# Optimization experiments

Hardware: AMD Instinct MI355X
Metric: run time of the kernel (lower is better)

Reference implementation:

```python
import jax, jax.numpy as jnp
import numpy as np

N_HEADS = 16
DIMS = 1024
HEAD_SIZE = DIMS // N_HEADS


def setup_inputs() -> dict:
    key = jax.random.key(0)
    k1, k2, k3, k4, k5 = jax.random.split(key, 5)
    x = jax.random.normal(k1, (1, 4096, DIMS), dtype=jnp.float32)
    s = 1.0 / np.sqrt(DIMS)
    w_qkv = jax.random.uniform(k2, (3 * DIMS, DIMS), jnp.float32, -s, s)
    b_qkv = jax.random.uniform(k3, (3 * DIMS,), jnp.float32, -s, s)
    w_o = jax.random.uniform(k4, (DIMS, DIMS), jnp.float32, -s, s)
    b_o = jax.random.uniform(k5, (DIMS,), jnp.float32, -s, s)
    return {"x": x, "w_qkv": w_qkv, "b_qkv": b_qkv, "w_o": w_o, "b_o": b_o,
            "causal_mask": 1}


def reference(x, w_qkv, b_qkv, w_o, b_o, causal_mask):
    B, S, D = x.shape
    qkv = x @ w_qkv.T + b_qkv                      # [B,S,3D]
    q, k, v = jnp.split(qkv, 3, axis=-1)
    def heads(t):
        return t.reshape(B, S, N_HEADS, HEAD_SIZE).transpose(0, 2, 1, 3)  # [B,H,S,hd]
    q, k, v = heads(q), heads(k), heads(v)
    scores = jnp.einsum("bhsd,bhtd->bhst", q, k)   # [B,H,S,S]
    if causal_mask:
        tri = jnp.triu(jnp.ones((S, S), dtype=bool), k=1)
        scores = jnp.where(tri, -jnp.inf, scores)  # mask BEFORE scale, as in torch code
    scores = scores / np.sqrt(HEAD_SIZE)
    weights = jax.nn.softmax(scores, axis=-1)
    out = jnp.einsum("bhst,bhtd->bhsd", weights, v)  # [B,H,S,hd]
    out = out.transpose(0, 2, 1, 3).reshape(B, S, D)
    return out @ w_o.T + b_o
```

## Files before the change

### kernel.cpp

```cpp
#include <hip/hip_runtime.h>
#include <hip/hip_bf16.h>
#include <stdint.h>

typedef __attribute__((ext_vector_type(8))) short short8;
typedef __attribute__((ext_vector_type(4))) float f32x4;
typedef __attribute__((ext_vector_type(16))) float f32x16;
typedef __attribute__((ext_vector_type(2))) unsigned int uint2u;
typedef __hip_bfloat16 bf16;

#define S_LEN 4096
#define DMODEL 1024
#define NH 16
#define HD 64
#define QSCALE 0.1803368801111f

static __device__ inline uint2 pack4(float4 v) {
  union { uint2 u; bf16 h[4]; } p;
  p.h[0] = (bf16)v.x; p.h[1] = (bf16)v.y; p.h[2] = (bf16)v.z; p.h[3] = (bf16)v.w;
  return p.u;
}

static __device__ inline uint32_t pack2(float a, float b) {
  union { uint32_t u; bf16 h[2]; } p;
  p.h[0] = (bf16)a; p.h[1] = (bf16)b;
  return p.u;
}

static __device__ inline float b2f(short s) {
  union { short s; bf16 h; } u; u.s = s; return (float)u.h;
}

static __device__ inline void gload_lds16(const bf16* g, bf16* l) {
  __builtin_amdgcn_global_load_lds(
      (const __attribute__((address_space(1))) unsigned int*)g,
      (__attribute__((address_space(3))) unsigned int*)l, 16, 0, 0);
}

static __device__ inline int rot_idx(int r, int c) {
  return r * 64 + ((c + ((r & 7) << 3)) & 63);
}

__global__ __launch_bounds__(256)
void cvt_all(const float* __restrict__ x, const float* __restrict__ wq,
             const float* __restrict__ wo, bf16* __restrict__ xb,
             bf16* __restrict__ wqb, bf16* __restrict__ wob) {
  const int nx = S_LEN * DMODEL;
  const int nq = 3 * DMODEL * DMODEL;
  const int no = DMODEL * DMODEL;
  int i = (blockIdx.x * 256 + threadIdx.x) * 4;
  if (i < nx) {
    *(uint2*)(xb + i) = pack4(*(const float4*)(x + i));
  } else if (i < nx + nq) {
    int j = i - nx;
    *(uint2*)(wqb + j) = pack4(*(const float4*)(wq + j));
  } else if (i < nx + nq + no) {
    int j = i - nx - nq;
    *(uint2*)(wob + j) = pack4(*(const float4*)(wo + j));
  }
}

__global__ __launch_bounds__(256)
void gemm_qkv(const bf16* __restrict__ A, const bf16* __restrict__ B,
              const float* __restrict__ bias, bf16* __restrict__ qkv2,
              bf16* __restrict__ vt) {
  const int K = DMODEL;
  __shared__ bf16 sA[128 * 64];
  __shared__ bf16 sB[128 * 64];
  const int tid  = threadIdx.x;
  const int lane = tid & 63;
  const int wave = tid >> 6;
  const int wm = wave >> 1, wn = wave & 1;
  const int tileM = blockIdx.y * 128;
  const int tileN = blockIdx.x * 128;

  const int lrow = lane & 15;
  const int quad = lane >> 4;
  const int kq   = quad * 8;

  f32x4 acc[4][4];
#pragma unroll
  for (int i = 0; i < 4; i++)
#pragma unroll
    for (int j = 0; j < 4; j++) acc[i][j] = (f32x4){0.f, 0.f, 0.f, 0.f};

  const int trl = lane >> 3;
  const int cgl = (((lane & 7) - trl) & 7) << 3;
  const bf16* aP[4];
  const bf16* bP[4];
#pragma unroll
  for (int c = 0; c < 4; c++) {
    int ch = wave * 4 + c;
    aP[c] = A + (size_t)(tileM + ch * 8 + trl) * K + cgl;
    bP[c] = B + (size_t)(tileN + ch * 8 + trl) * K + cgl;
  }

  for (int k0 = 0; k0 < K; k0 += 64) {
    __syncthreads();
#pragma unroll
    for (int c = 0; c < 4; c++) {
      int ch = wave * 4 + c;
      gload_lds16(aP[c] + k0, sA + ch * 512);
      gload_lds16(bP[c] + k0, sB + ch * 512);
    }
    __syncthreads();
#pragma unroll
    for (int ks = 0; ks < 2; ks++) {
      short8 afrag[4], bfrag[4];
#pragma unroll
      for (int mi = 0; mi < 4; mi++)
        afrag[mi] = *(const short8*)(sA + rot_idx(wm * 64 + mi * 16 + lrow, ks * 32 + kq));
#pragma unroll
      for (int ni = 0; ni < 4; ni++)
        bfrag[ni] = *(const short8*)(sB + rot_idx(wn * 64 + ni * 16 + lrow, ks * 32 + kq));
#pragma unroll
      for (int mi = 0; mi < 4; mi++)
#pragma unroll
        for (int ni = 0; ni < 4; ni++)
          acc[mi][ni] = __builtin_amdgcn_mfma_f32_16x16x32_bf16(afrag[mi], bfrag[ni], acc[mi][ni], 0, 0, 0);
    }
  }

#pragma unroll
  for (int ni = 0; ni < 4; ni++) {
    int col = tileN + wn * 64 + ni * 16 + lrow;
    float bv = bias[col];
    if (col < 2 * DMODEL) {
      float sc = (col < DMODEL) ? QSCALE : 1.0f;
#pragma unroll
      for (int mi = 0; mi < 4; mi++) {
        int row0 = tileM + wm * 64 + mi * 16 + quad * 4;
#pragma unroll
        for (int r = 0; r < 4; r++)
          qkv2[(size_t)(row0 + r) * 2048 + col] = (bf16)((acc[mi][ni][r] + bv) * sc);
      }
    } else {
      int cc = col - 2 * DMODEL;
      int hh = cc >> 6, dd = cc & 63;
      bf16* vrow = vt + ((size_t)(hh * 64 + dd)) * S_LEN;
#pragma unroll
      for (int mi = 0; mi < 4; mi++) {
        int row0 = tileM + wm * 64 + mi * 16 + quad * 4;
        float4 v = {acc[mi][ni][0] + bv, acc[mi][ni][1] + bv,
                    acc[mi][ni][2] + bv, acc[mi][ni][3] + bv};
        *(uint2*)(vrow + row0) = pack4(v);
      }
    }
  }
}

__global__ __launch_bounds__(256)
void gemm_oproj(const bf16* __restrict__ A, const bf16* __restrict__ B,
                const float* __restrict__ bias, float* __restrict__ C) {
  const int K = DMODEL, N = DMODEL;
  __shared__ bf16 sA[128 * 64];
  __shared__ bf16 sB[64 * 64];
  const int tid  = threadIdx.x;
  const int lane = tid & 63;
  const int wave = tid >> 6;
  const int wm = wave >> 1, wn = wave & 1;
  const int tileM = blockIdx.y * 128;
  const int tileN = blockIdx.x * 64;

  const int lrow = lane & 15;
  const int quad = lane >> 4;
  const int kq   = quad * 8;

  f32x4 acc[4][2];
#pragma unroll
  for (int i = 0; i < 4; i++)
#pragma unroll
    for (int j = 0; j < 2; j++) acc[i][j] = (f32x4){0.f, 0.f, 0.f, 0.f};

  const int trl = lane >> 3;
  const int cgl = (((lane & 7) - trl) & 7) << 3;
  const bf16* aP[4];
  const bf16* bP[2];
#pragma unroll
  for (int c = 0; c < 4; c++) {
    int ch = wave * 4 + c;
    aP[c] = A + (size_t)(tileM + ch * 8 + trl) * K + cgl;
  }
#pragma unroll
  for (int c = 0; c < 2; c++) {
    int ch = wave * 2 + c;
    bP[c] = B + (size_t)(tileN + ch * 8 + trl) * K + cgl;
  }

  for (int k0 = 0; k0 < K; k0 += 64) {
    __syncthreads();
#pragma unroll
    for (int c = 0; c < 4; c++)
      gload_lds16(aP[c] + k0, sA + (wave * 4 + c) * 512);
#pragma unroll
    for (int c = 0; c < 2; c++)
      gload_lds16(bP[c] + k0, sB + (wave * 2 + c) * 512);
    __syncthreads();
#pragma unroll
    for (int ks = 0; ks < 2; ks++) {
      short8 afrag[4], bfrag[2];
#pragma unroll
      for (int mi = 0; mi < 4; mi++)
        afrag[mi] = *(const short8*)(sA + rot_idx(wm * 64 + mi * 16 + lrow, ks * 32 + kq));
#pragma unroll
      for (int ni = 0; ni < 2; ni++)
        bfrag[ni] = *(const short8*)(sB + rot_idx(wn * 32 + ni * 16 + lrow, ks * 32 + kq));
#pragma unroll
      for (int mi = 0; mi < 4; mi++)
#pragma unroll
        for (int ni = 0; ni < 2; ni++)
          acc[mi][ni] = __builtin_amdgcn_mfma_f32_16x16x32_bf16(afrag[mi], bfrag[ni], acc[mi][ni], 0, 0, 0);
    }
  }

#pragma unroll
  for (int ni = 0; ni < 2; ni++) {
    int col = tileN + wn * 32 + ni * 16 + lrow;
    float bv = bias[col];
#pragma unroll
    for (int mi = 0; mi < 4; mi++) {
      int row0 = tileM + wm * 64 + mi * 16 + quad * 4;
#pragma unroll
      for (int r = 0; r < 4; r++)
        C[(size_t)(row0 + r) * N + col] = acc[mi][ni][r] + bv;
    }
  }
}

__global__ __launch_bounds__(256)
void gemm_qkv_f32(const float* __restrict__ A, const float* __restrict__ B,
                  const float* __restrict__ bias, bf16* __restrict__ qkv2,
                  bf16* __restrict__ vt) {
  const int K = DMODEL;
  __shared__ bf16 sA[128 * 64];
  __shared__ bf16 sB[128 * 64];
  const int tid  = threadIdx.x;
  const int lane = tid & 63;
  const int wave = tid >> 6;
  const int wm = wave >> 1, wn = wave & 1;
  const int tileM = blockIdx.y * 128;
  const int tileN = blockIdx.x * 128;
  const int lrow = lane & 15;
  const int quad = lane >> 4;
  const int kq   = quad * 8;

  f32x4 acc[4][4];
#pragma unroll
  for (int i = 0; i < 4; i++)
#pragma unroll
    for (int j = 0; j < 4; j++) acc[i][j] = (f32x4){0.f, 0.f, 0.f, 0.f};

  const int r0 = tid >> 4;
  const int cc = (tid & 15) * 4;

  for (int k0 = 0; k0 < K; k0 += 64) {
    uint2 ra[8], rb[8];
#pragma unroll
    for (int i = 0; i < 8; i++) {
      int row = r0 + i * 16;
      ra[i] = pack4(*(const float4*)(A + (size_t)(tileM + row) * K + k0 + cc));
      rb[i] = pack4(*(const float4*)(B + (size_t)(tileN + row) * K + k0 + cc));
    }
    __syncthreads();
#pragma unroll
    for (int i = 0; i < 8; i++) {
      int row = r0 + i * 16;
      *(uint2*)(sA + row * 64 + cc) = ra[i];
      *(uint2*)(sB + row * 64 + cc) = rb[i];
    }
    __syncthreads();
#pragma unroll
    for (int ks = 0; ks < 2; ks++) {
      short8 afrag[4], bfrag[4];
#pragma unroll
      for (int mi = 0; mi < 4; mi++)
        afrag[mi] = *(const short8*)(sA + (wm * 64 + mi * 16 + lrow) * 64 + ks * 32 + kq);
#pragma unroll
      for (int ni = 0; ni < 4; ni++)
        bfrag[ni] = *(const short8*)(sB + (wn * 64 + ni * 16 + lrow) * 64 + ks * 32 + kq);
#pragma unroll
      for (int mi = 0; mi < 4; mi++)
#pragma unroll
        for (int ni = 0; ni < 4; ni++)
          acc[mi][ni] = __builtin_amdgcn_mfma_f32_16x16x32_bf16(afrag[mi], bfrag[ni], acc[mi][ni], 0, 0, 0);
    }
  }
#pragma unroll
  for (int ni = 0; ni < 4; ni++) {
    int col = tileN + wn * 64 + ni * 16 + lrow;
    float bv = bias[col];
    if (col < 2 * DMODEL) {
      float sc = (col < DMODEL) ? QSCALE : 1.0f;
#pragma unroll
      for (int mi = 0; mi < 4; mi++) {
        int row0 = tileM + wm * 64 + mi * 16 + quad * 4;
#pragma unroll
        for (int r = 0; r < 4; r++)
          qkv2[(size_t)(row0 + r) * 2048 + col] = (bf16)((acc[mi][ni][r] + bv) * sc);
      }
    } else {
      int c2 = col - 2 * DMODEL;
      int hh = c2 >> 6, dd = c2 & 63;
      bf16* vrow = vt + ((size_t)(hh * 64 + dd)) * S_LEN;
#pragma unroll
      for (int mi = 0; mi < 4; mi++) {
        int row0 = tileM + wm * 64 + mi * 16 + quad * 4;
        float4 v = {acc[mi][ni][0] + bv, acc[mi][ni][1] + bv,
                    acc[mi][ni][2] + bv, acc[mi][ni][3] + bv};
        *(uint2*)(vrow + row0) = pack4(v);
      }
    }
  }
}

__global__ __launch_bounds__(256)
void gemm_oproj_f32w(const bf16* __restrict__ A, const float* __restrict__ B,
                     const float* __restrict__ bias, float* __restrict__ C) {
  const int K = DMODEL, N = DMODEL;
  __shared__ bf16 sA[128 * 64];
  __shared__ bf16 sB[128 * 64];
  const int tid  = threadIdx.x;
  const int lane = tid & 63;
  const int wave = tid >> 6;
  const int wm = wave >> 1, wn = wave & 1;
  const int tileM = blockIdx.y * 128;
  const int tileN = blockIdx.x * 128;
  const int lrow = lane & 15;
  const int quad = lane >> 4;
  const int kq   = quad * 8;

  f32x4 acc[4][4];
#pragma unroll
  for (int i = 0; i < 4; i++)
#pragma unroll
    for (int j = 0; j < 4; j++) acc[i][j] = (f32x4){0.f, 0.f, 0.f, 0.f};

  const int a_r0 = tid >> 3;
  const int a_cc = (tid & 7) * 8;
  const int b_r0 = tid >> 4;
  const int b_cc = (tid & 15) * 4;

  for (int k0 = 0; k0 < K; k0 += 64) {
    uint4 ra[4];
    uint2 rb[8];
#pragma unroll
    for (int i = 0; i < 4; i++)
      ra[i] = *(const uint4*)(A + (size_t)(tileM + a_r0 + i * 32) * K + k0 + a_cc);
#pragma unroll
    for (int i = 0; i < 8; i++)
      rb[i] = pack4(*(const float4*)(B + (size_t)(tileN + b_r0 + i * 16) * K + k0 + b_cc));
    __syncthreads();
#pragma unroll
    for (int i = 0; i < 4; i++)
      *(uint4*)(sA + (a_r0 + i * 32) * 64 + a_cc) = ra[i];
#pragma unroll
    for (int i = 0; i < 8; i++)
      *(uint2*)(sB + (b_r0 + i * 16) * 64 + b_cc) = rb[i];
    __syncthreads();
#pragma unroll
    for (int ks = 0; ks < 2; ks++) {
      short8 afrag[4], bfrag[4];
#pragma unroll
      for (int mi = 0; mi < 4; mi++)
        afrag[mi] = *(const short8*)(sA + (wm * 64 + mi * 16 + lrow) * 64 + ks * 32 + kq);
#pragma unroll
      for (int ni = 0; ni < 4; ni++)
        bfrag[ni] = *(const short8*)(sB + (wn * 64 + ni * 16 + lrow) * 64 + ks * 32 + kq);
#pragma unroll
      for (int mi = 0; mi < 4; mi++)
#pragma unroll
        for (int ni = 0; ni < 4; ni++)
          acc[mi][ni] = __builtin_amdgcn_mfma_f32_16x16x32_bf16(afrag[mi], bfrag[ni], acc[mi][ni], 0, 0, 0);
    }
  }
#pragma unroll
  for (int ni = 0; ni < 4; ni++) {
    int col = tileN + wn * 64 + ni * 16 + lrow;
    float bv = bias[col];
#pragma unroll
    for (int mi = 0; mi < 4; mi++) {
      int row0 = tileM + wm * 64 + mi * 16 + quad * 4;
#pragma unroll
      for (int r = 0; r < 4; r++)
        C[(size_t)(row0 + r) * N + col] = acc[mi][ni][r] + bv;
    }
  }
}

__global__ __launch_bounds__(256, 4)
void attn_kernel(const bf16* __restrict__ qkv2, const bf16* __restrict__ vt,
                 bf16* __restrict__ attn_out, const int* __restrict__ causal_ptr,
                 bf16* __restrict__ p0, bf16* __restrict__ p1,
                 bf16* __restrict__ p2) {
  __shared__ bf16 smem[2][64 * 64];
  __shared__ float lbuf[64];

  const int tid  = threadIdx.x;
  const int lane = tid & 63;
  const int wave = tid >> 6;
  const int qh   = wave >> 1;
  const int kh   = wave & 1;

  const int id   = blockIdx.y * 192 + blockIdx.x;
  const int xcd  = id & 7;
  const int hh   = (id >> 3) & 1;
  const int h    = xcd + (hh << 3);
  const int rest = id >> 4;
  const int rank = rest / 3;
  const int ck   = rest - rank * 3;
  const int qi   = 63 - rank;
  const int qbase = qi * 64;
  const bool causal = (*causal_ptr) != 0;

  const int l31 = lane & 31;
  const int hi  = lane >> 5;
  const int trl = lane >> 3;
  const int cgl = (((lane & 7) - trl) & 7) << 3;

  const bf16* Qb = qkv2 + h * HD;
  const bf16* Kb = qkv2 + DMODEL + h * HD;
  const bf16* Vb = vt + (size_t)(h * HD) * S_LEN;

  bf16* const A = smem[0];
  bf16* const B = smem[1];

  const int Lt  = causal ? (qi + 1) : (S_LEN / 64);
  const int jt0 = (Lt * ck) / 3;
  const int jt1 = (Lt * (ck + 1)) / 3;

  const int wrmin = qbase + qh * 32;
  const int wrmax = wrmin + 31;
  const int q_g   = wrmin + l31;

  if (jt0 < jt1) {
#pragma unroll
    for (int i = 0; i < 2; i++) {
      int ch = wave * 2 + i;
      int trow = ch * 8 + trl;
      gload_lds16(Kb + (size_t)(jt0 * 64 + trow) * 2048 + cgl, A + ch * 512);
      gload_lds16(Vb + (size_t)trow * S_LEN + jt0 * 64 + cgl, B + ch * 512);
    }
  }
  short8 qf[4];
#pragma unroll
  for (int kd = 0; kd < 4; kd++)
    qf[kd] = *(const short8*)(Qb + (size_t)q_g * 2048 + kd * 16 + hi * 8);

  f32x16 oacc[2];
#pragma unroll
  for (int nc = 0; nc < 2; nc++)
#pragma unroll
    for (int e = 0; e < 16; e++) oacc[nc][e] = 0.f;
  float l_st = 0.f;

  __syncthreads();

  for (int jt = jt0; jt < jt1; jt++) {
    const int kbase = jt * 64;
    const int kh32 = kbase + kh * 32;
    const bool live = !(causal && kh32 > wrmax);

    uint32_t pw[2][4];
    if (live) {
      f32x16 sacc;
#pragma unroll
      for (int e = 0; e < 16; e++) sacc[e] = 0.f;
      __builtin_amdgcn_s_setprio(1);
#pragma unroll
      for (int kd = 0; kd < 4; kd++) {
        short8 kf = *(const short8*)(A + rot_idx(kh * 32 + l31, kd * 16 + hi * 8));
        sacc = __builtin_amdgcn_mfma_f32_32x32x16_bf16(kf, qf[kd], sacc, 0, 0, 0);
      }
      __builtin_amdgcn_s_setprio(0);
      const bool nm = causal && (kh32 + 31 > wrmin);
      uint32_t pku[4][2];
      float psum = 0.f;
#pragma unroll
      for (int g = 0; g < 4; g++) {
#pragma unroll
        for (int h2 = 0; h2 < 2; h2++) {
          float v0 = __builtin_amdgcn_exp2f(sacc[g * 4 + h2 * 2]);
          float v1 = __builtin_amdgcn_exp2f(sacc[g * 4 + h2 * 2 + 1]);
          if (nm) {
            int kg = kh32 + g * 8 + hi * 4 + h2 * 2;
            if (kg > q_g)     v0 = 0.f;
            if (kg + 1 > q_g) v1 = 0.f;
          }
          psum += v0 + v1;
          pku[g][h2] = pack2(v0, v1);
        }
      }
      l_st += psum;
#pragma unroll
      for (int c2 = 0; c2 < 2; c2++) {
#pragma unroll
        for (int h2 = 0; h2 < 2; h2++) {
          uint2u sw = __builtin_amdgcn_permlane32_swap(
              pku[2 * c2][h2], pku[2 * c2 + 1][h2], false, false);
          pw[c2][h2]     = sw[0];
          pw[c2][2 + h2] = sw[1];
        }
      }
    }

    __syncthreads();

    if (jt + 1 < jt1) {
      const int kb2 = kbase + 64;
#pragma unroll
      for (int i = 0; i < 2; i++) {
        int ch = wave * 2 + i;
        int trow = ch * 8 + trl;
        gload_lds16(Kb + (size_t)(kb2 + trow) * 2048 + cgl, A + ch * 512);
      }
    }

    if (live) {
      __builtin_amdgcn_s_setprio(1);
#pragma unroll
      for (int c2 = 0; c2 < 2; c2++) {
        if (causal && (kh32 + c2 * 16 > wrmax)) continue;
        union { short8 s; uint32_t u[4]; } pf;
#pragma unroll
        for (int w = 0; w < 4; w++) pf.u[w] = pw[c2][w];
#pragma unroll
        for (int nc = 0; nc < 2; nc++) {
          short8 vf = *(const short8*)(B +
              rot_idx(nc * 32 + l31, (kh * 2 + c2) * 16 + hi * 8));
          oacc[nc] = __builtin_amdgcn_mfma_f32_32x32x16_bf16(pf.s, vf, oacc[nc], 0, 0, 0);
        }
      }
      __builtin_amdgcn_s_setprio(0);
    }

    __syncthreads();

    if (jt + 1 < jt1) {
      const int kb2 = kbase + 64;
#pragma unroll
      for (int i = 0; i < 2; i++) {
        int ch = wave * 2 + i;
        int trow = ch * 8 + trl;
        gload_lds16(Vb + (size_t)trow * S_LEN + kb2 + cgl, B + ch * 512);
      }
    }
  }

  float ltot = l_st + __shfl_xor(l_st, 32);
  float* obuf = (float*)smem;
  if (kh == 1) {
    float* ob = obuf + qh * 2048;
#pragma unroll
    for (int nc = 0; nc < 2; nc++)
#pragma unroll
      for (int e = 0; e < 16; e++)
        ob[(nc * 16 + e) * 64 + lane] = oacc[nc][e];
    if (hi == 0) lbuf[qh * 32 + l31] = ltot;
  }
  __syncthreads();
  if (kh == 0) {
    float* ob = obuf + qh * 2048;
#pragma unroll
    for (int nc = 0; nc < 2; nc++)
#pragma unroll
      for (int e = 0; e < 16; e++)
        oacc[nc][e] += ob[(nc * 16 + e) * 64 + lane];
    ltot += lbuf[qh * 32 + l31];

    if (hi == 0) {
      float* lrow = (float*)(attn_out +
          (size_t)(qbase + ck * 2 + qh) * DMODEL + h * HD);
      lrow[l31] = ltot;
    }
    bf16* po = (ck == 0 ? p0 : (ck == 1 ? p1 : p2)) +
               (size_t)(h * 64 + qi) * 4096;
#pragma unroll
    for (int nc = 0; nc < 2; nc++)
#pragma unroll
      for (int g = 0; g < 4; g++)
#pragma unroll
        for (int r = 0; r < 4; r++)
          po[(qh * 32 + g * 8 + hi * 4 + r) * 64 + nc * 32 + l31] =
              (bf16)oacc[nc][g * 4 + r];
  }
}

__global__ __launch_bounds__(256)
void attn_merge(const bf16* __restrict__ p0, const bf16* __restrict__ p1,
                const bf16* __restrict__ p2, bf16* __restrict__ attn_out) {
  const int qi = blockIdx.x;
  const int h  = blockIdx.y;
  const int tid = threadIdx.x;
  const int qbase = qi * 64;
  __shared__ float lsh[192];
  if (tid < 192) {
    int ckv  = tid >> 6;
    int qhv  = (tid >> 5) & 1;
    int l31v = tid & 31;
    const float* lrow = (const float*)(attn_out +
        (size_t)(qbase + ckv * 2 + qhv) * DMODEL + h * HD);
    lsh[tid] = lrow[l31v];
  }
  __syncthreads();

  const int q  = tid >> 2;
  const int d0 = (tid & 3) * 16;
  const float linv = 1.0f / fmaxf(lsh[q] + lsh[64 + q] + lsh[128 + q], 1e-30f);
  const size_t slot = (size_t)(h * 64 + qi) * 4096 + q * 64 + d0;
  short8 x0 = *(const short8*)(p0 + slot);
  short8 x1 = *(const short8*)(p0 + slot + 8);
  short8 y0 = *(const short8*)(p1 + slot);
  short8 y1 = *(const short8*)(p1 + slot + 8);
  short8 z0 = *(const short8*)(p2 + slot);
  short8 z1 = *(const short8*)(p2 + slot + 8);
  uint32_t w[8];
#pragma unroll
  for (int j = 0; j < 4; j++) {
    float a = (b2f(x0[2 * j]) + b2f(y0[2 * j]) + b2f(z0[2 * j])) * linv;
    float b = (b2f(x0[2 * j + 1]) + b2f(y0[2 * j + 1]) + b2f(z0[2 * j + 1])) * linv;
    w[j] = pack2(a, b);
  }
#pragma unroll
  for (int j = 0; j < 4; j++) {
    float a = (b2f(x1[2 * j]) + b2f(y1[2 * j]) + b2f(z1[2 * j])) * linv;
    float b = (b2f(x1[2 * j + 1]) + b2f(y1[2 * j + 1]) + b2f(z1[2 * j + 1])) * linv;
    w[4 + j] = pack2(a, b);
  }
  bf16* outp = attn_out + (size_t)(qbase + q) * DMODEL + h * HD + d0;
  *(uint4*)(outp)     = (uint4){w[0], w[1], w[2], w[3]};
  *(uint4*)(outp + 8) = (uint4){w[4], w[5], w[6], w[7]};
}

extern "C" void kernel_launch(void* const* d_in, const int* in_sizes, int n_in,
                              void* d_out, int out_size, void* d_ws, size_t ws_size,
                              hipStream_t stream) {
  const float* x     = (const float*)d_in[0];
  const float* w_qkv = (const float*)d_in[1];
  const float* b_qkv = (const float*)d_in[2];
  const float* w_o   = (const float*)d_in[3];
  const float* b_o   = (const float*)d_in[4];
  const int*   cm    = (const int*)d_in[5];

  char* ws = (char*)d_ws;
  bf16* qkv2 = (bf16*)ws;
  bf16* vt   = (bf16*)(ws + 16777216);
  bf16* attn = (bf16*)(ws + 25165824);
  bf16* xb   = (bf16*)(ws + 33554432);
  bf16* wqb  = (bf16*)(ws + 41943040);
  bf16* wob  = (bf16*)(ws + 48234496);

  bf16* p0 = (bf16*)d_out;
  bf16* p1 = (bf16*)d_out + 4194304;
  bf16* p2 = (bf16*)(ws + 33554432);

  dim3 blk(256);
  const bool fast = (ws_size >= (size_t)50331648);

  if (fast) {
    const int ntot = S_LEN * DMODEL + 3 * DMODEL * DMODEL + DMODEL * DMODEL;
    cvt_all<<<dim3((ntot / 4 + 255) / 256), blk, 0, stream>>>(
        x, w_qkv, w_o, xb, wqb, wob);
    gemm_qkv<<<dim3(3 * DMODEL / 128, S_LEN / 128), blk, 0, stream>>>(
        xb, wqb, b_qkv, qkv2, vt);
    attn_kernel<<<dim3(192, NH), blk, 0, stream>>>(qkv2, vt, attn, cm,
                                                   p0, p1, p2);
    attn_merge<<<dim3(64, NH), blk, 0, stream>>>(p0, p1, p2, attn);
    gemm_oproj<<<dim3(DMODEL / 64, S_LEN / 128), blk, 0, stream>>>(
        attn, wob, b_o, (float*)d_out);
  } else {
    gemm_qkv_f32<<<dim3(3 * DMODEL / 128, S_LEN / 128), blk, 0, stream>>>(
        x, w_qkv, b_qkv, qkv2, vt);
    attn_kernel<<<dim3(192, NH), blk, 0, stream>>>(qkv2, vt, attn, cm,
                                                   p0, p1, p2);
    attn_merge<<<dim3(64, NH), blk, 0, stream>>>(p0, p1, p2, attn);
    gemm_oproj_f32w<<<dim3(DMODEL / 128, S_LEN / 128), blk, 0, stream>>>(
        attn, w_o, b_o, (float*)d_out);
  }
}
```

Baseline: 207.3 us.

## Double-buffer K/V tiles in attention and widen o-proj GEMM tile to 128x128

The attention kernel now keeps two LDS buffers each for K and V. It prefetches the next tile at the start of each iteration, which removes one of the two barriers per iteration and overlaps global loads with compute. Separately, the output-projection GEMM tile grows from 128x64 to 128x128 to get more reuse per block. This doubles attention LDS use (32KB), which may lower occupancy under launch_bounds(256,4). The o-proj grid also drops to 256 blocks, which may underfill the GPU.

Result: no change. 210.9 us (+1.7%).

```diff
diff --git a/kernel.cpp b/kernel.cpp
--- a/kernel.cpp
+++ b/kernel.cpp
@@ -153,68 +153,64 @@
                 const float* __restrict__ bias, float* __restrict__ C) {
   const int K = DMODEL, N = DMODEL;
   __shared__ bf16 sA[128 * 64];
-  __shared__ bf16 sB[64 * 64];
+  __shared__ bf16 sB[128 * 64];
   const int tid  = threadIdx.x;
   const int lane = tid & 63;
   const int wave = tid >> 6;
   const int wm = wave >> 1, wn = wave & 1;
   const int tileM = blockIdx.y * 128;
-  const int tileN = blockIdx.x * 64;
+  const int tileN = blockIdx.x * 128;
 
   const int lrow = lane & 15;
   const int quad = lane >> 4;
   const int kq   = quad * 8;
 
-  f32x4 acc[4][2];
+  f32x4 acc[4][4];
 #pragma unroll
   for (int i = 0; i < 4; i++)
 #pragma unroll
-    for (int j = 0; j < 2; j++) acc[i][j] = (f32x4){0.f, 0.f, 0.f, 0.f};
+    for (int j = 0; j < 4; j++) acc[i][j] = (f32x4){0.f, 0.f, 0.f, 0.f};
 
   const int trl = lane >> 3;
   const int cgl = (((lane & 7) - trl) & 7) << 3;
   const bf16* aP[4];
-  const bf16* bP[2];
+  const bf16* bP[4];
 #pragma unroll
   for (int c = 0; c < 4; c++) {
     int ch = wave * 4 + c;
     aP[c] = A + (size_t)(tileM + ch * 8 + trl) * K + cgl;
-  }
-#pragma unroll
-  for (int c = 0; c < 2; c++) {
-    int ch = wave * 2 + c;
     bP[c] = B + (size_t)(tileN + ch * 8 + trl) * K + cgl;
   }
 
   for (int k0 = 0; k0 < K; k0 += 64) {
     __syncthreads();
 #pragma unroll
-    for (int c = 0; c < 4; c++)
-      gload_lds16(aP[c] + k0, sA + (wave * 4 + c) * 512);
-#pragma unroll
-    for (int c = 0; c < 2; c++)
-      gload_lds16(bP[c] + k0, sB + (wave * 2 + c) * 512);
+    for (int c = 0; c < 4; c++) {
+      int ch = wave * 4 + c;
+      gload_lds16(aP[c] + k0, sA + ch * 512);
+      gload_lds16(bP[c] + k0, sB + ch * 512);
+    }
     __syncthreads();
 #pragma unroll
     for (int ks = 0; ks < 2; ks++) {
-      short8 afrag[4], bfrag[2];
+      short8 afrag[4], bfrag[4];
 #pragma unroll
       for (int mi = 0; mi < 4; mi++)
         afrag[mi] = *(const short8*)(sA + rot_idx(wm * 64 + mi * 16 + lrow, ks * 32 + kq));
 #pragma unroll
-      for (int ni = 0; ni < 2; ni++)
-        bfrag[ni] = *(const short8*)(sB + rot_idx(wn * 32 + ni * 16 + lrow, ks * 32 + kq));
-#pragma unroll
-      for (int mi = 0; mi < 4; mi++)
-#pragma unroll
-        for (int ni = 0; ni < 2; ni++)
+      for (int ni = 0; ni < 4; ni++)
+        bfrag[ni] = *(const short8*)(sB + rot_idx(wn * 64 + ni * 16 + lrow, ks * 32 + kq));
+#pragma unroll
+      for (int mi = 0; mi < 4; mi++)
+#pragma unroll
+        for (int ni = 0; ni < 4; ni++)
           acc[mi][ni] = __builtin_amdgcn_mfma_f32_16x16x32_bf16(afrag[mi], bfrag[ni], acc[mi][ni], 0, 0, 0);
     }
   }
 
 #pragma unroll
-  for (int ni = 0; ni < 2; ni++) {
-    int col = tileN + wn * 32 + ni * 16 + lrow;
+  for (int ni = 0; ni < 4; ni++) {
+    int col = tileN + wn * 64 + ni * 16 + lrow;
     float bv = bias[col];
 #pragma unroll
     for (int mi = 0; mi < 4; mi++) {
@@ -391,7 +387,8 @@
                  bf16* __restrict__ attn_out, const int* __restrict__ causal_ptr,
                  bf16* __restrict__ p0, bf16* __restrict__ p1,
                  bf16* __restrict__ p2) {
-  __shared__ bf16 smem[2][64 * 64];
+  __shared__ bf16 sK[2][64 * 64];
+  __shared__ bf16 sV[2][64 * 64];
   __shared__ float lbuf[64];
 
   const int tid  = threadIdx.x;
@@ -420,9 +417,6 @@
   const bf16* Kb = qkv2 + DMODEL + h * HD;
   const bf16* Vb = vt + (size_t)(h * HD) * S_LEN;
 
-  bf16* const A = smem[0];
-  bf16* const B = smem[1];
-
   const int Lt  = causal ? (qi + 1) : (S_LEN / 64);
   const int jt0 = (Lt * ck) / 3;
   const int jt1 = (Lt * (ck + 1)) / 3;
@@ -436,8 +430,8 @@
     for (int i = 0; i < 2; i++) {
       int ch = wave * 2 + i;
       int trow = ch * 8 + trl;
-      gload_lds16(Kb + (size_t)(jt0 * 64 + trow) * 2048 + cgl, A + ch * 512);
-      gload_lds16(Vb + (size_t)trow * S_LEN + jt0 * 64 + cgl, B + ch * 512);
+      gload_lds16(Kb + (size_t)(jt0 * 64 + trow) * 2048 + cgl, sK[0] + ch * 512);
+      gload_lds16(Vb + (size_t)trow * S_LEN + jt0 * 64 + cgl, sV[0] + ch * 512);
     }
   }
   short8 qf[4];
@@ -455,11 +449,22 @@
   __syncthreads();
 
   for (int jt = jt0; jt < jt1; jt++) {
+    const int cur = (jt - jt0) & 1;
     const int kbase = jt * 64;
     const int kh32 = kbase + kh * 32;
     const bool live = !(causal && kh32 > wrmax);
 
-    uint32_t pw[2][4];
+    if (jt + 1 < jt1) {
+      const int kb2 = kbase + 64;
+#pragma unroll
+      for (int i = 0; i < 2; i++) {
+        int ch = wave * 2 + i;
+        int trow = ch * 8 + trl;
+        gload_lds16(Kb + (size_t)(kb2 + trow) * 2048 + cgl, sK[cur ^ 1] + ch * 512);
+        gload_lds16(Vb + (size_t)trow * S_LEN + kb2 + cgl, sV[cur ^ 1] + ch * 512);
+      }
+    }
+
     if (live) {
       f32x16 sacc;
 #pragma unroll
@@ -467,7 +472,7 @@
       __builtin_amdgcn_s_setprio(1);
 #pragma unroll
       for (int kd = 0; kd < 4; kd++) {
-        short8 kf = *(const short8*)(A + rot_idx(kh * 32 + l31, kd * 16 + hi * 8));
+        short8 kf = *(const short8*)(sK[cur] + rot_idx(kh * 32 + l31, kd * 16 + hi * 8));
         sacc = __builtin_amdgcn_mfma_f32_32x32x16_bf16(kf, qf[kd], sacc, 0, 0, 0);
       }
       __builtin_amdgcn_s_setprio(0);
@@ -490,6 +495,7 @@
         }
       }
       l_st += psum;
+      uint32_t pw[2][4];
 #pragma unroll
       for (int c2 = 0; c2 < 2; c2++) {
 #pragma unroll
@@ -500,21 +506,7 @@
           pw[c2][2 + h2] = sw[1];
         }
       }
-    }
-
-    __syncthreads();
-
-    if (jt + 1 < jt1) {
-      const int kb2 = kbase + 64;
-#pragma unroll
-      for (int i = 0; i < 2; i++) {
-        int ch = wave * 2 + i;
-        int trow = ch * 8 + trl;
-        gload_lds16(Kb + (size_t)(kb2 + trow) * 2048 + cgl, A + ch * 512);
-      }
-    }
-
-    if (live) {
+
       __builtin_amdgcn_s_setprio(1);
 #pragma unroll
       for (int c2 = 0; c2 < 2; c2++) {
@@ -524,7 +516,7 @@
         for (int w = 0; w < 4; w++) pf.u[w] = pw[c2][w];
 #pragma unroll
         for (int nc = 0; nc < 2; nc++) {
-          short8 vf = *(const short8*)(B +
+          short8 vf = *(const short8*)(sV[cur] +
               rot_idx(nc * 32 + l31, (kh * 2 + c2) * 16 + hi * 8));
           oacc[nc] = __builtin_amdgcn_mfma_f32_32x32x16_bf16(pf.s, vf, oacc[nc], 0, 0, 0);
         }
@@ -533,20 +525,10 @@
     }
 
     __syncthreads();
-
-    if (jt + 1 < jt1) {
-      const int kb2 = kbase + 64;
-#pragma unroll
-      for (int i = 0; i < 2; i++) {
-        int ch = wave * 2 + i;
-        int trow = ch * 8 + trl;
-        gload_lds16(Vb + (size_t)trow * S_LEN + kb2 + cgl, B + ch * 512);
-      }
-    }
   }
 
   float ltot = l_st + __shfl_xor(l_st, 32);
-  float* obuf = (float*)smem;
+  float* obuf = (float*)sK;
   if (kh == 1) {
     float* ob = obuf + qh * 2048;
 #pragma unroll
@@ -664,7 +646,7 @@
     attn_kernel<<<dim3(192, NH), blk, 0, stream>>>(qkv2, vt, attn, cm,
                                                    p0, p1, p2);
     attn_merge<<<dim3(64, NH), blk, 0, stream>>>(p0, p1, p2, attn);
-    gemm_oproj<<<dim3(DMODEL / 64, S_LEN / 128), blk, 0, stream>>>(
+    gemm_oproj<<<dim3(DMODEL / 128, S_LEN / 128), blk, 0, stream>>>(
         attn, wob, b_o, (float*)d_out);
   } else {
     gemm_qkv_f32<<<dim3(3 * DMODEL / 128, S_LEN / 128), blk, 0, stream>>>(
```

## Double-buffer K/V tiles in attention and swizzle GEMM block order across XCDs

Applied to the files above, without the earlier changes.

The attention loop now keeps two LDS buffers each for K and V and issues the next tile's loads at the top of each iteration. This cuts the barriers per iteration from two to one, so global-to-LDS traffic overlaps the QK and PV MFMA work. The price is twice the LDS per block (32KB instead of 16KB), which may lower occupancy under the 4-blocks-per-CU launch bound. The QKV and output-projection GEMMs also remap block IDs so that consecutive blocks on the same XCD touch neighbouring tiles, aiming for better L2 reuse.

Result: no change. 207.6 us (+0.1%).

```diff
diff --git a/kernel.cpp b/kernel.cpp
--- a/kernel.cpp
+++ b/kernel.cpp
@@ -70,8 +70,11 @@
   const int lane = tid & 63;
   const int wave = tid >> 6;
   const int wm = wave >> 1, wn = wave & 1;
-  const int tileM = blockIdx.y * 128;
-  const int tileN = blockIdx.x * 128;
+
+  const int id0 = blockIdx.y * 24 + blockIdx.x;
+  const int swz = (id0 & 7) * 96 + (id0 >> 3);
+  const int tileM = (swz / 24) * 128;
+  const int tileN = (swz % 24) * 128;
 
   const int lrow = lane & 15;
   const int quad = lane >> 4;
@@ -158,8 +161,11 @@
   const int lane = tid & 63;
   const int wave = tid >> 6;
   const int wm = wave >> 1, wn = wave & 1;
-  const int tileM = blockIdx.y * 128;
-  const int tileN = blockIdx.x * 64;
+
+  const int id0 = blockIdx.y * 16 + blockIdx.x;
+  const int swz = (id0 & 7) * 64 + (id0 >> 3);
+  const int tileM = (swz / 16) * 128;
+  const int tileN = (swz % 16) * 64;
 
   const int lrow = lane & 15;
   const int quad = lane >> 4;
@@ -391,7 +397,8 @@
                  bf16* __restrict__ attn_out, const int* __restrict__ causal_ptr,
                  bf16* __restrict__ p0, bf16* __restrict__ p1,
                  bf16* __restrict__ p2) {
-  __shared__ bf16 smem[2][64 * 64];
+  __shared__ bf16 sK[2][64 * 64];
+  __shared__ bf16 sV[2][64 * 64];
   __shared__ float lbuf[64];
 
   const int tid  = threadIdx.x;
@@ -420,9 +427,6 @@
   const bf16* Kb = qkv2 + DMODEL + h * HD;
   const bf16* Vb = vt + (size_t)(h * HD) * S_LEN;
 
-  bf16* const A = smem[0];
-  bf16* const B = smem[1];
-
   const int Lt  = causal ? (qi + 1) : (S_LEN / 64);
   const int jt0 = (Lt * ck) / 3;
   const int jt1 = (Lt * (ck + 1)) / 3;
@@ -431,13 +435,23 @@
   const int wrmax = wrmin + 31;
   const int q_g   = wrmin + l31;
 
+  const bf16* kC[2];
+  const bf16* vC[2];
+#pragma unroll
+  for (int i = 0; i < 2; i++) {
+    int trow = (wave * 2 + i) * 8 + trl;
+    kC[i] = Kb + (size_t)trow * 2048 + cgl;
+    vC[i] = Vb + (size_t)trow * S_LEN + cgl;
+  }
+
   if (jt0 < jt1) {
+    const size_t k0off = (size_t)jt0 * (64 * 2048);
+    const int    v0off = jt0 * 64;
 #pragma unroll
     for (int i = 0; i < 2; i++) {
       int ch = wave * 2 + i;
-      int trow = ch * 8 + trl;
-      gload_lds16(Kb + (size_t)(jt0 * 64 + trow) * 2048 + cgl, A + ch * 512);
-      gload_lds16(Vb + (size_t)trow * S_LEN + jt0 * 64 + cgl, B + ch * 512);
+      gload_lds16(kC[i] + k0off, sK[0] + ch * 512);
+      gload_lds16(vC[i] + v0off, sV[0] + ch * 512);
     }
   }
   short8 qf[4];
@@ -454,12 +468,26 @@
 
   __syncthreads();
 
+  size_t kOff = (size_t)(jt0 + 1) * (64 * 2048);
+  int    vOff = (jt0 + 1) * 64;
+
   for (int jt = jt0; jt < jt1; jt++) {
+    const int cur = (jt - jt0) & 1;
     const int kbase = jt * 64;
     const int kh32 = kbase + kh * 32;
     const bool live = !(causal && kh32 > wrmax);
 
-    uint32_t pw[2][4];
+    if (jt + 1 < jt1) {
+#pragma unroll
+      for (int i = 0; i < 2; i++) {
+        int ch = wave * 2 + i;
+        gload_lds16(kC[i] + kOff, sK[cur ^ 1] + ch * 512);
+        gload_lds16(vC[i] + vOff, sV[cur ^ 1] + ch * 512);
+      }
+    }
+    kOff += 64 * 2048;
+    vOff += 64;
+
     if (live) {
       f32x16 sacc;
 #pragma unroll
@@ -467,7 +495,7 @@
       __builtin_amdgcn_s_setprio(1);
 #pragma unroll
       for (int kd = 0; kd < 4; kd++) {
-        short8 kf = *(const short8*)(A + rot_idx(kh * 32 + l31, kd * 16 + hi * 8));
+        short8 kf = *(const short8*)(sK[cur] + rot_idx(kh * 32 + l31, kd * 16 + hi * 8));
         sacc = __builtin_amdgcn_mfma_f32_32x32x16_bf16(kf, qf[kd], sacc, 0, 0, 0);
       }
       __builtin_amdgcn_s_setprio(0);
@@ -490,6 +518,7 @@
         }
       }
       l_st += psum;
+      uint32_t pw[2][4];
 #pragma unroll
       for (int c2 = 0; c2 < 2; c2++) {
 #pragma unroll
@@ -500,21 +529,7 @@
           pw[c2][2 + h2] = sw[1];
         }
       }
-    }
-
-    __syncthreads();
-
-    if (jt + 1 < jt1) {
-      const int kb2 = kbase + 64;
-#pragma unroll
-      for (int i = 0; i < 2; i++) {
-        int ch = wave * 2 + i;
-        int trow = ch * 8 + trl;
-        gload_lds16(Kb + (size_t)(kb2 + trow) * 2048 + cgl, A + ch * 512);
-      }
-    }
-
-    if (live) {
+
       __builtin_amdgcn_s_setprio(1);
 #pragma unroll
       for (int c2 = 0; c2 < 2; c2++) {
@@ -524,7 +539,7 @@
         for (int w = 0; w < 4; w++) pf.u[w] = pw[c2][w];
 #pragma unroll
         for (int nc = 0; nc < 2; nc++) {
-          short8 vf = *(const short8*)(B +
+          short8 vf = *(const short8*)(sV[cur] +
               rot_idx(nc * 32 + l31, (kh * 2 + c2) * 16 + hi * 8));
           oacc[nc] = __builtin_amdgcn_mfma_f32_32x32x16_bf16(pf.s, vf, oacc[nc], 0, 0, 0);
         }
@@ -533,20 +548,10 @@
     }
 
     __syncthreads();
-
-    if (jt + 1 < jt1) {
-      const int kb2 = kbase + 64;
-#pragma unroll
-      for (int i = 0; i < 2; i++) {
-        int ch = wave * 2 + i;
-        int trow = ch * 8 + trl;
-        gload_lds16(Vb + (size_t)trow * S_LEN + kb2 + cgl, B + ch * 512);
-      }
-    }
   }
 
   float ltot = l_st + __shfl_xor(l_st, 32);
-  float* obuf = (float*)smem;
+  float* obuf = (float*)sK;
   if (kh == 1) {
     float* ob = obuf + qh * 2048;
 #pragma unroll
```
